# Performance work log

Measured on AMD Instinct MI355X. Metric: run time of the kernel, lower is better.

The kernel has to match this reference:

```python
import jax, jax.numpy as jnp
import numpy as np

# dims
B, N, D = 256, 77, 768     # batch, CLIP tokens, token dim
K, Dn, H = 16, 768, 8      # nodes, node dim, heads
HID, L = 512, 2            # edge-MLP hidden, num GNN layers


def setup_inputs() -> dict:
    key = jax.random.key(0)
    ks = jax.random.split(key, 12)
    g = lambda k, shape, s=0.02: (jax.random.normal(k, shape, jnp.float32) * s)
    return {
        "w": jax.random.normal(ks[0], (B, N, D), jnp.float32),
        "token_mask": jax.random.randint(ks[1], (B, N), 0, 2).astype(jnp.int32),
        "node_queries": g(ks[2], (1, K, Dn)),
        "Wq": g(ks[3], (Dn, Dn)), "bq": jnp.zeros((Dn,), jnp.float32),
        "Wk": g(ks[4], (D, Dn)),  "bk": jnp.zeros((Dn,), jnp.float32),
        "Wv": g(ks[5], (D, Dn)),  "bv": jnp.zeros((Dn,), jnp.float32),
        "We1": g(ks[6], (2 * Dn, HID)), "be1": jnp.zeros((HID,), jnp.float32),
        "We2": g(ks[7], (HID, 1)),      "be2": jnp.zeros((1,), jnp.float32),
        "fuse_gate": jnp.float32(0.0),
        "Wg": g(ks[8], (L, Dn, Dn)), "bg": jnp.zeros((L, Dn), jnp.float32),
    }


def _edge_logits(V, We1, be1, We2, be2):
    # edge_mlp(cat[Vi, Vj]) without materializing [B,K,K,2Dn]:
    # split first linear into the Vi-half and Vj-half of its weight.
    hi = V @ We1[:Dn]   # [B,K,HID]
    hj = V @ We1[Dn:]   # [B,K,HID]
    h = jax.nn.relu(hi[:, :, None, :] + hj[:, None, :, :] + be1)  # [B,K,K,HID]
    return jnp.einsum('bijh,h->bij', h, We2[:, 0]) + be2[0]       # [B,K,K]


def _forward(w, node_queries, Wq, bq, Wk, bk, Wv, bv,
             We1, be1, We2, be2, fuse_gate, Wg, bg, token_mask):
    q = jnp.broadcast_to(node_queries, (B, K, Dn))
    Q = q @ Wq + bq        # [B,K,Dn]
    Kt = w @ Wk + bk       # [B,N,Dn]
    Vt = w @ Wv + bv       # [B,N,Dn]
    # per-head dot products summed over heads == full Dn dot product
    scale = (Dn // H) ** -0.5
    scores = jnp.einsum('bkd,bnd->bkn', Q, Kt) * scale  # [B,K,N]
    pad = (token_mask == 0)[:, None, :]                 # [B,1,N]
    scores = jnp.where(pad, jnp.finfo(scores.dtype).min, scores)
    # softmax over K per token (transpose to [B,N,K])
    S = jax.nn.softmax(jnp.swapaxes(scores, 1, 2), axis=-1)  # [B,N,K]
    V = jnp.einsum('bnk,bnd->bkd', S, Vt)                    # [B,K,Dn]
    gate = jax.nn.sigmoid(fuse_gate)
    V = (1.0 - gate) * V + gate * q
    # pre-GNN edge logits, then relational GNN refinement
    E = _edge_logits(V, We1, be1, We2, be2)
    A = jax.nn.softmax(E, axis=-1)  # [B,K,K], fixed across layers
    for l in range(L):
        msg = jnp.einsum('bij,bjd->bid', A, V @ Wg[l] + bg[l])
        V = V + jax.nn.relu(msg)
    # post-GNN edge logits
    E = _edge_logits(V, We1, be1, We2, be2)
    return S, V, E


def reference(w, token_mask, node_queries, Wq, bq, Wk, bk, Wv, bv,
              We1, be1, We2, be2, fuse_gate, Wg, bg):
    return _forward(w, node_queries, Wq, bq, Wk, bk, Wv, bv,
                    We1, be1, We2, be2, fuse_gate, Wg, bg, token_mask)
```

## Files before the change

kernel.cpp:

```cpp
#include <hip/hip_runtime.h>

typedef unsigned short u16;
typedef __attribute__((ext_vector_type(8))) short short8;
typedef __attribute__((ext_vector_type(4))) float f32x4;

#define DEV static __device__ __forceinline__

DEV float bf2f(u16 u) { return __uint_as_float(((unsigned)u) << 16); }
DEV u16 f2bf(float f) {
  unsigned u = __float_as_uint(f);
  return (u16)((u + 0x7fffu + ((u >> 16) & 1u)) >> 16);
}

DEV void cp16(void* lds, const void* g) {
  __builtin_amdgcn_global_load_lds(
      (const __attribute__((address_space(1))) unsigned int*)g,
      (__attribute__((address_space(3))) unsigned int*)lds, 16, 0, 0);
}


__global__ __launch_bounds__(256) void tcast_all(const float* __restrict__ Wv,
                                                 const float* __restrict__ We1,
                                                 const float* __restrict__ Wg,
                                                 u16* __restrict__ WvT,
                                                 u16* __restrict__ We1T,
                                                 u16* __restrict__ WgT) {
  __shared__ float tile[32][33];
  const float* src; u16* dst; int C;
  switch (blockIdx.z) {
    case 0: src = Wv;           dst = WvT;           C = 768; break;
    case 1: src = We1;          dst = We1T;          C = 512; break;
    case 2: src = We1 + 393216; dst = We1T + 393216; C = 512; break;
    case 3: src = Wg;           dst = WgT;           C = 768; break;
    default: src = Wg + 589824; dst = WgT + 589824;  C = 768; break;
  }
  int r0 = blockIdx.y * 32, c0 = blockIdx.x * 32;
  if (c0 >= C) return;
  int tr = threadIdx.x >> 5, tc = threadIdx.x & 31;
#pragma unroll
  for (int rr = 0; rr < 4; ++rr)
    tile[tr + rr * 8][tc] = src[(size_t)(r0 + tr + rr * 8) * C + c0 + tc];
  __syncthreads();
#pragma unroll
  for (int rr = 0; rr < 4; ++rr)
    dst[(size_t)(c0 + tr + rr * 8) * 768 + r0 + tc] = f2bf(tile[tc][tr + rr * 8]);
}

__global__ __launch_bounds__(256) void q_part(const float* __restrict__ nq,
                                              const float* __restrict__ Wq,
                                              float* __restrict__ Qpart) {
  int gid = blockIdx.x * 256 + threadIdx.x;
  int s = blockIdx.y;
  int k = gid / 768, d = gid % 768;
  const float* nr = nq + k * 768 + s * 96;
  const float* wp = Wq + (size_t)(s * 96) * 768 + d;
  float s0 = 0.f, s1 = 0.f, s2 = 0.f, s3 = 0.f;
#pragma unroll
  for (int c = 0; c < 96; c += 4) {
    s0 += nr[c + 0] * wp[(size_t)(c + 0) * 768];
    s1 += nr[c + 1] * wp[(size_t)(c + 1) * 768];
    s2 += nr[c + 2] * wp[(size_t)(c + 2) * 768];
    s3 += nr[c + 3] * wp[(size_t)(c + 3) * 768];
  }
  Qpart[(size_t)s * 12288 + gid] = (s0 + s1) + (s2 + s3);
}

__global__ __launch_bounds__(256) void q_reduce(const float* __restrict__ Qpart,
                                                const float* __restrict__ bq,
                                                float* __restrict__ Qf) {
  int gid = blockIdx.x * 256 + threadIdx.x;
  int d = gid % 768;
  float s = bq[d];
#pragma unroll
  for (int i = 0; i < 8; ++i) s += Qpart[(size_t)i * 12288 + gid];
  Qf[gid] = s;
}

__global__ __launch_bounds__(256) void pt_kernel(const float* __restrict__ Qf,
                                                 const float* __restrict__ Wk,
                                                 const float* __restrict__ bk,
                                                 u16* __restrict__ PT16,
                                                 float* __restrict__ qb) {
  int t = threadIdx.x;
  if (blockIdx.x == 48) {
    int k = t >> 4, j = t & 15;
    const float* q = Qf + k * 768 + j * 48;
    const float* bp = bk + j * 48;
    float s = 0.f;
#pragma unroll
    for (int d = 0; d < 48; d += 4) {
      f32x4 qv = *(const f32x4*)&q[d];
      f32x4 bv4 = *(const f32x4*)&bp[d];
      s += qv[0] * bv4[0] + qv[1] * bv4[1] + qv[2] * bv4[2] + qv[3] * bv4[3];
    }
#pragma unroll
    for (int off = 1; off < 16; off <<= 1) s += __shfl_xor(s, off);
    if (j == 0) qb[k] = s;
    return;
  }
  int gid = blockIdx.x * 256 + t;
  int c = gid >> 4, k = gid & 15;
  const float* wr = Wk + (size_t)c * 768;
  const float* q = Qf + k * 768;
  float s = 0.f;
  for (int d = 0; d < 768; d += 4) {
    f32x4 wv = *(const f32x4*)&wr[d];
    f32x4 qv = *(const f32x4*)&q[d];
    s += wv[0] * qv[0] + wv[1] * qv[1] + wv[2] * qv[2] + wv[3] * qv[3];
  }
  PT16[k * 768 + c] = f2bf(s);
}

__global__ __launch_bounds__(256) void scoreu_kernel(const float* __restrict__ w,
                                                     const u16* __restrict__ PT16,
                                                     const float* __restrict__ qb,
                                                     const int* __restrict__ mask,
                                                     float* __restrict__ Sout,
                                                     u16* __restrict__ U16,
                                                     float* __restrict__ sk) {
  __shared__ u16 Ps[16 * 776];
  __shared__ float Ss[80 * 16];
  int b = blockIdx.x, t = threadIdx.x;
  int wave = t >> 6, lane = t & 63, l16 = lane & 15, quad = lane >> 4;
#pragma unroll
  for (int r = 0; r < 6; ++r) {
    int idx = t + 256 * r;
    int row = idx / 96, c8 = idx % 96;
    *(short8*)&Ps[row * 776 + c8 * 8] = *(const short8*)&PT16[row * 768 + c8 * 8];
  }
  __syncthreads();
  const float scale = 0.1020620726159658f;
  float qv = qb[l16];
  for (int tile = wave; tile < 5; tile += 4) {
    int nrow = tile * 16 + l16;
    int nclamp = nrow < 77 ? nrow : 76;
    const float* ap = w + ((size_t)b * 77 + nclamp) * 768 + quad * 8;
    f32x4 acc = {0.f, 0.f, 0.f, 0.f};
#pragma unroll
    for (int it = 0; it < 24; ++it) {
      f32x4 a0 = *(const f32x4*)(ap + it * 32);
      f32x4 a1 = *(const f32x4*)(ap + it * 32 + 4);
      short8 fa;
#pragma unroll
      for (int e = 0; e < 4; ++e) { fa[e] = (short)f2bf(a0[e]); fa[e + 4] = (short)f2bf(a1[e]); }
      short8 fb = *(const short8*)&Ps[l16 * 776 + it * 32 + quad * 8];
      acc = __builtin_amdgcn_mfma_f32_16x16x32_bf16(fa, fb, acc, 0, 0, 0);
    }
#pragma unroll
    for (int r = 0; r < 4; ++r) {
      int n_r = tile * 16 + quad * 4 + r;
      if (n_r < 77) {
        float s = (acc[r] + qv) * scale;
        if (mask[b * 77 + n_r] == 0) s = -3.402823466e38f;
        float mx = s;
#pragma unroll
        for (int off = 1; off < 16; off <<= 1) mx = fmaxf(mx, __shfl_xor(mx, off));
        float e = __expf(s - mx);
        float sm = e;
#pragma unroll
        for (int off = 1; off < 16; off <<= 1) sm += __shfl_xor(sm, off);
        float p = e / sm;
        Sout[((size_t)b * 77 + n_r) * 16 + l16] = p;
        Ss[n_r * 16 + l16] = p;
      }
    }
  }
  __syncthreads();
  float a0[16], a1[16], a2[16];
#pragma unroll
  for (int k = 0; k < 16; ++k) { a0[k] = 0.f; a1[k] = 0.f; a2[k] = 0.f; }
  const float* wb = w + (size_t)b * 59136;
  for (int n = 0; n < 77; ++n) {
    const float* wr = wb + (size_t)n * 768;
    float w0 = wr[t], w1 = wr[t + 256], w2 = wr[t + 512];
    const float* sr = &Ss[n * 16];
#pragma unroll
    for (int k = 0; k < 16; ++k) {
      float s = sr[k];
      a0[k] += s * w0; a1[k] += s * w1; a2[k] += s * w2;
    }
  }
  u16* ub = U16 + (size_t)b * 12288;
#pragma unroll
  for (int k = 0; k < 16; ++k) {
    ub[k * 768 + t] = f2bf(a0[k]);
    ub[k * 768 + t + 256] = f2bf(a1[k]);
    ub[k * 768 + t + 512] = f2bf(a2[k]);
  }
  if (t < 16) {
    float s = 0.f;
    for (int n = 0; n < 77; ++n) s += Ss[n * 16 + t];
    sk[b * 16 + t] = s;
  }
}

__global__ __launch_bounds__(256) void vgemm(const u16* __restrict__ A,
                                             const u16* __restrict__ BT,
                                             const float* __restrict__ skp,
                                             const float* __restrict__ bv,
                                             const float* __restrict__ nq,
                                             const float* __restrict__ gatep,
                                             float* __restrict__ V32,
                                             u16* __restrict__ V16) {
  __shared__ u16 As[2 * 64 * 32];
  __shared__ u16 Bs[2 * 128 * 32];
  int mi = blockIdx.x / 6, ni = blockIdx.x % 6;
  int m0 = mi * 64, n0 = ni * 128;
  int t = threadIdx.x;
  int wave = t >> 6, lane = t & 63, l16 = lane & 15, quad = lane >> 4;
  int ra = wave * 16 + (lane >> 2);
  int rb1 = wave * 32 + (lane >> 2);
  int rb2 = rb1 + 16;
  int cslot = lane & 3;
  int cga = (cslot ^ ((ra >> 1) & 3)) * 8;
  int cgb1 = (cslot ^ ((rb1 >> 1) & 3)) * 8;
  int cgb2 = (cslot ^ ((rb2 >> 1) & 3)) * 8;

  const u16* Ap = A + (size_t)(m0 + ra) * 768 + cga;
  const u16* Bp1 = BT + (size_t)(n0 + rb1) * 768 + cgb1;
  const u16* Bp2 = BT + (size_t)(n0 + rb2) * 768 + cgb2;
  u16* AsW = &As[(wave * 16) * 32];
  u16* BsW1 = &Bs[(wave * 32) * 32];
  u16* BsW2 = &Bs[(wave * 32 + 16) * 32];

  f32x4 zero4 = {0.f, 0.f, 0.f, 0.f};
  f32x4 acc[4][2];
#pragma unroll
  for (int i = 0; i < 4; ++i) { acc[i][0] = zero4; acc[i][1] = zero4; }

  cp16(AsW, Ap); cp16(BsW1, Bp1); cp16(BsW2, Bp2);

  int cur = 0;
  for (int k0 = 0; k0 < 768; k0 += 32) {
    int nxt = cur ^ 1;
    if (k0 + 32 < 768) {
      cp16(AsW + nxt * 2048, Ap + k0 + 32);
      cp16(BsW1 + nxt * 4096, Bp1 + k0 + 32);
      cp16(BsW2 + nxt * 4096, Bp2 + k0 + 32);
      asm volatile("s_waitcnt vmcnt(3)" ::: "memory");
    } else {
      asm volatile("s_waitcnt vmcnt(0)" ::: "memory");
    }
    asm volatile("s_barrier" ::: "memory");
    const u16* Ab = &As[cur * 2048];
    const u16* Bb = &Bs[cur * 4096];
    short8 fa[4], fb[2];
#pragma unroll
    for (int i = 0; i < 4; ++i) {
      int R = i * 16 + l16;
      fa[i] = *(const short8*)&Ab[R * 32 + (quad ^ ((R >> 1) & 3)) * 8];
    }
#pragma unroll
    for (int j = 0; j < 2; ++j) {
      int R = wave * 32 + j * 16 + l16;
      fb[j] = *(const short8*)&Bb[R * 32 + (quad ^ ((R >> 1) & 3)) * 8];
    }
#pragma unroll
    for (int i = 0; i < 4; ++i)
#pragma unroll
      for (int j = 0; j < 2; ++j)
        acc[i][j] = __builtin_amdgcn_mfma_f32_16x16x32_bf16(fa[i], fb[j], acc[i][j], 0, 0, 0);
    asm volatile("s_barrier" ::: "memory");
    cur = nxt;
  }

  float gv = gatep[0];
  float g = 1.f / (1.f + __expf(-gv)), og = 1.f - g;
  int narr[2]; float bvj[2];
#pragma unroll
  for (int j = 0; j < 2; ++j) {
    narr[j] = n0 + wave * 32 + j * 16 + l16;
    bvj[j] = bv[narr[j]];
  }
#pragma unroll
  for (int i = 0; i < 4; ++i)
#pragma unroll
    for (int r = 0; r < 4; ++r) {
      int m = m0 + i * 16 + quad * 4 + r;
      float skv = skp[m];
      size_t mrow = (size_t)m * 768;
      const float* nqr = nq + (m & 15) * 768;
#pragma unroll
      for (int j = 0; j < 2; ++j) {
        float val = acc[i][j][r] + skv * bvj[j];
        float v = og * val + g * nqr[narr[j]];
        V32[mrow + narr[j]] = v;
        V16[mrow + narr[j]] = f2bf(v);
      }
    }
}

__global__ __launch_bounds__(256) void gemm16s(const u16* __restrict__ A,
                                               const u16* __restrict__ BT0,
                                               const float* __restrict__ bias0,
                                               u16* __restrict__ C0, int N0, int ntA,
                                               const u16* __restrict__ BT1,
                                               const float* __restrict__ bias1,
                                               u16* __restrict__ C1, int N1, int ntB,
                                               int K) {
  __shared__ u16 As[2 * 64 * 32];
  __shared__ u16 Bs[2 * 128 * 32];
  int nt = ntA + ntB;
  int mi = blockIdx.x / nt, ni = blockIdx.x % nt;
  const u16* BT; const float* bias; u16* C; int N, n0;
  if (ni < ntA) { BT = BT0; bias = bias0; C = C0; N = N0; n0 = ni * 128; }
  else          { BT = BT1; bias = bias1; C = C1; N = N1; n0 = (ni - ntA) * 128; }
  int m0 = mi * 64;
  int t = threadIdx.x;
  int wave = t >> 6, lane = t & 63, l16 = lane & 15, quad = lane >> 4;
  int ra = wave * 16 + (lane >> 2);
  int rb1 = wave * 32 + (lane >> 2);
  int rb2 = rb1 + 16;
  int cslot = lane & 3;
  int cga = (cslot ^ ((ra >> 1) & 3)) * 8;
  int cgb1 = (cslot ^ ((rb1 >> 1) & 3)) * 8;
  int cgb2 = (cslot ^ ((rb2 >> 1) & 3)) * 8;

  const u16* Ap = A + (size_t)(m0 + ra) * K + cga;
  const u16* Bp1 = BT + (size_t)(n0 + rb1) * K + cgb1;
  const u16* Bp2 = BT + (size_t)(n0 + rb2) * K + cgb2;
  u16* AsW = &As[(wave * 16) * 32];
  u16* BsW1 = &Bs[(wave * 32) * 32];
  u16* BsW2 = &Bs[(wave * 32 + 16) * 32];

  f32x4 zero4 = {0.f, 0.f, 0.f, 0.f};
  f32x4 acc[4][2];
#pragma unroll
  for (int i = 0; i < 4; ++i) { acc[i][0] = zero4; acc[i][1] = zero4; }

  cp16(AsW, Ap); cp16(BsW1, Bp1); cp16(BsW2, Bp2);

  int cur = 0;
  for (int k0 = 0; k0 < K; k0 += 32) {
    int nxt = cur ^ 1;
    if (k0 + 32 < K) {
      cp16(AsW + nxt * 2048, Ap + k0 + 32);
      cp16(BsW1 + nxt * 4096, Bp1 + k0 + 32);
      cp16(BsW2 + nxt * 4096, Bp2 + k0 + 32);
      asm volatile("s_waitcnt vmcnt(3)" ::: "memory");
    } else {
      asm volatile("s_waitcnt vmcnt(0)" ::: "memory");
    }
    asm volatile("s_barrier" ::: "memory");
    const u16* Ab = &As[cur * 2048];
    const u16* Bb = &Bs[cur * 4096];
    short8 fa[4], fb[2];
#pragma unroll
    for (int i = 0; i < 4; ++i) {
      int R = i * 16 + l16;
      fa[i] = *(const short8*)&Ab[R * 32 + (quad ^ ((R >> 1) & 3)) * 8];
    }
#pragma unroll
    for (int j = 0; j < 2; ++j) {
      int R = wave * 32 + j * 16 + l16;
      fb[j] = *(const short8*)&Bb[R * 32 + (quad ^ ((R >> 1) & 3)) * 8];
    }
#pragma unroll
    for (int i = 0; i < 4; ++i)
#pragma unroll
      for (int j = 0; j < 2; ++j)
        acc[i][j] = __builtin_amdgcn_mfma_f32_16x16x32_bf16(fa[i], fb[j], acc[i][j], 0, 0, 0);
    asm volatile("s_barrier" ::: "memory");
    cur = nxt;
  }

  int narr[2]; float bvj[2];
#pragma unroll
  for (int j = 0; j < 2; ++j) {
    narr[j] = n0 + wave * 32 + j * 16 + l16;
    bvj[j] = bias ? bias[narr[j]] : 0.f;
  }
#pragma unroll
  for (int i = 0; i < 4; ++i)
#pragma unroll
    for (int r = 0; r < 4; ++r) {
      size_t mrow = (size_t)(m0 + i * 16 + quad * 4 + r) * N;
#pragma unroll
      for (int j = 0; j < 2; ++j)
        C[mrow + narr[j]] = f2bf(acc[i][j][r] + bvj[j]);
    }
}

__global__ __launch_bounds__(256) void edge_kernel(const u16* __restrict__ HIJ,
                                                   const float* __restrict__ be1,
                                                   const float* __restrict__ We2,
                                                   const float* __restrict__ be2v,
                                                   float* __restrict__ Aout,
                                                   float* __restrict__ Eout) {
  __shared__ float hiS[16 * 260];
  __shared__ float hjS[16 * 260];
  __shared__ float be1s[512];
  __shared__ float w2s[512];
  int b = blockIdx.x, t = threadIdx.x;
  be1s[t] = be1[t]; be1s[t + 256] = be1[t + 256];
  w2s[t] = We2[t];  w2s[t + 256] = We2[t + 256];

  int i = t >> 4, jj = t & 15;
  float e = 0.f;
  for (int half = 0; half < 2; ++half) {
    __syncthreads();
#pragma unroll
    for (int r = 0; r < 2; ++r) {
      int idx = t + 256 * r;
      int row = idx >> 5, c8 = idx & 31;
      const u16* src = &HIJ[(size_t)(b * 16 + row) * 1024 + half * 256 + c8 * 8];
      short8 hv = *(const short8*)src;
      short8 jv = *(const short8*)(src + 512);
      f32x4 l0, l1, m0v, m1v;
#pragma unroll
      for (int ee = 0; ee < 4; ++ee) {
        l0[ee] = bf2f((u16)hv[ee]); l1[ee] = bf2f((u16)hv[ee + 4]);
        m0v[ee] = bf2f((u16)jv[ee]); m1v[ee] = bf2f((u16)jv[ee + 4]);
      }
      *(f32x4*)&hiS[row * 260 + c8 * 8] = l0;
      *(f32x4*)&hiS[row * 260 + c8 * 8 + 4] = l1;
      *(f32x4*)&hjS[row * 260 + c8 * 8] = m0v;
      *(f32x4*)&hjS[row * 260 + c8 * 8 + 4] = m1v;
    }
    __syncthreads();
    const float* hi = &hiS[i * 260];
    const float* hj = &hjS[jj * 260];
    const float* b1 = &be1s[half * 256];
    const float* w2 = &w2s[half * 256];
#pragma unroll 2
    for (int h4 = 0; h4 < 64; ++h4) {
      f32x4 hv = *(const f32x4*)&hi[h4 * 4];
      f32x4 jv = *(const f32x4*)&hj[h4 * 4];
      f32x4 bv = *(const f32x4*)&b1[h4 * 4];
      f32x4 wv = *(const f32x4*)&w2[h4 * 4];
#pragma unroll
      for (int ee = 0; ee < 4; ++ee)
        e += fmaxf(hv[ee] + jv[ee] + bv[ee], 0.f) * wv[ee];
    }
  }
  e += be2v[0];

  if (Aout) {
    float mx = e;
#pragma unroll
    for (int off = 1; off < 16; off <<= 1) mx = fmaxf(mx, __shfl_xor(mx, off));
    float ex = __expf(e - mx);
    float sm = ex;
#pragma unroll
    for (int off = 1; off < 16; off <<= 1) sm += __shfl_xor(sm, off);
    Aout[(size_t)b * 256 + t] = ex / sm;
  }
  if (Eout) Eout[(size_t)b * 256 + t] = e;
}

__global__ __launch_bounds__(256) void edgecombine_kernel(const u16* __restrict__ HIJ,
                                                          const float* __restrict__ be1,
                                                          const float* __restrict__ We2,
                                                          const float* __restrict__ be2v,
                                                          float* __restrict__ Aout,
                                                          const u16* __restrict__ G,
                                                          float* __restrict__ V32,
                                                          u16* __restrict__ V16) {
  __shared__ float buf[16 * 772];
  __shared__ float be1s[512];
  __shared__ float w2s[512];
  __shared__ float As_s[256];
  float* hiS = buf;
  float* hjS = buf + 16 * 260;
  int b = blockIdx.x, t = threadIdx.x;
  be1s[t] = be1[t]; be1s[t + 256] = be1[t + 256];
  w2s[t] = We2[t];  w2s[t + 256] = We2[t + 256];

  int i = t >> 4, jj = t & 15;
  float e = 0.f;
  for (int half = 0; half < 2; ++half) {
    __syncthreads();
#pragma unroll
    for (int r = 0; r < 2; ++r) {
      int idx = t + 256 * r;
      int row = idx >> 5, c8 = idx & 31;
      const u16* src = &HIJ[(size_t)(b * 16 + row) * 1024 + half * 256 + c8 * 8];
      short8 hv = *(const short8*)src;
      short8 jv = *(const short8*)(src + 512);
      f32x4 l0, l1, m0v, m1v;
#pragma unroll
      for (int ee = 0; ee < 4; ++ee) {
        l0[ee] = bf2f((u16)hv[ee]); l1[ee] = bf2f((u16)hv[ee + 4]);
        m0v[ee] = bf2f((u16)jv[ee]); m1v[ee] = bf2f((u16)jv[ee + 4]);
      }
      *(f32x4*)&hiS[row * 260 + c8 * 8] = l0;
      *(f32x4*)&hiS[row * 260 + c8 * 8 + 4] = l1;
      *(f32x4*)&hjS[row * 260 + c8 * 8] = m0v;
      *(f32x4*)&hjS[row * 260 + c8 * 8 + 4] = m1v;
    }
    __syncthreads();
    const float* hi = &hiS[i * 260];
    const float* hj = &hjS[jj * 260];
    const float* b1 = &be1s[half * 256];
    const float* w2 = &w2s[half * 256];
#pragma unroll 2
    for (int h4 = 0; h4 < 64; ++h4) {
      f32x4 hv = *(const f32x4*)&hi[h4 * 4];
      f32x4 jv = *(const f32x4*)&hj[h4 * 4];
      f32x4 bv = *(const f32x4*)&b1[h4 * 4];
      f32x4 wv = *(const f32x4*)&w2[h4 * 4];
#pragma unroll
      for (int ee = 0; ee < 4; ++ee)
        e += fmaxf(hv[ee] + jv[ee] + bv[ee], 0.f) * wv[ee];
    }
  }
  e += be2v[0];

  float mx = e;
#pragma unroll
  for (int off = 1; off < 16; off <<= 1) mx = fmaxf(mx, __shfl_xor(mx, off));
  float ex = __expf(e - mx);
  float sm = ex;
#pragma unroll
  for (int off = 1; off < 16; off <<= 1) sm += __shfl_xor(sm, off);
  float p = ex / sm;
  As_s[t] = p;
  Aout[(size_t)b * 256 + t] = p;
  __syncthreads();

  float* Gs = buf;
#pragma unroll
  for (int r = 0; r < 6; ++r) {
    int idx = t + 256 * r;
    int row = idx / 96, c8 = idx % 96;
    short8 gv8 = *(const short8*)&G[(size_t)(b * 16 + row) * 768 + c8 * 8];
    f32x4 l0, l1;
#pragma unroll
    for (int ee = 0; ee < 4; ++ee) { l0[ee] = bf2f((u16)gv8[ee]); l1[ee] = bf2f((u16)gv8[ee + 4]); }
    *(f32x4*)&Gs[row * 772 + c8 * 8] = l0;
    *(f32x4*)&Gs[row * 772 + c8 * 8 + 4] = l1;
  }
  __syncthreads();
#pragma unroll
  for (int m = 0; m < 3; ++m) {
    int d = t + m * 256;
    float gv[16];
#pragma unroll
    for (int j = 0; j < 16; ++j) gv[j] = Gs[j * 772 + d];
#pragma unroll
    for (int ii = 0; ii < 16; ++ii) {
      float msg = 0.f;
#pragma unroll
      for (int j = 0; j < 16; ++j) msg += As_s[ii * 16 + j] * gv[j];
      size_t idx = (size_t)b * 12288 + (size_t)ii * 768 + d;
      float v = V32[idx] + fmaxf(msg, 0.f);
      V32[idx] = v;
      V16[idx] = f2bf(v);
    }
  }
}

__global__ __launch_bounds__(256) void combine_kernel(const float* __restrict__ Aws,
                                                      const u16* __restrict__ G,
                                                      float* __restrict__ V32,
                                                      u16* __restrict__ V16,
                                                      float* __restrict__ Vout) {
  __shared__ float Gs[16 * 772];
  __shared__ float As[256];
  int b = blockIdx.x, t = threadIdx.x;
#pragma unroll
  for (int r = 0; r < 6; ++r) {
    int idx = t + 256 * r;
    int row = idx / 96, c8 = idx % 96;
    short8 gv8 = *(const short8*)&G[(size_t)(b * 16 + row) * 768 + c8 * 8];
    f32x4 l0, l1;
#pragma unroll
    for (int ee = 0; ee < 4; ++ee) { l0[ee] = bf2f((u16)gv8[ee]); l1[ee] = bf2f((u16)gv8[ee + 4]); }
    *(f32x4*)&Gs[row * 772 + c8 * 8] = l0;
    *(f32x4*)&Gs[row * 772 + c8 * 8 + 4] = l1;
  }
  As[t] = Aws[(size_t)b * 256 + t];
  __syncthreads();
#pragma unroll
  for (int m = 0; m < 3; ++m) {
    int d = t + m * 256;
    float gv[16];
#pragma unroll
    for (int j = 0; j < 16; ++j) gv[j] = Gs[j * 772 + d];
#pragma unroll
    for (int i = 0; i < 16; ++i) {
      float msg = 0.f;
#pragma unroll
      for (int j = 0; j < 16; ++j) msg += As[i * 16 + j] * gv[j];
      size_t idx = (size_t)b * 12288 + (size_t)i * 768 + d;
      float v = V32[idx] + fmaxf(msg, 0.f);
      V32[idx] = v;
      V16[idx] = f2bf(v);
      if (Vout) Vout[idx] = v;
    }
  }
}

extern "C" void kernel_launch(void* const* d_in, const int* in_sizes, int n_in,
                              void* d_out, int out_size, void* d_ws, size_t ws_size,
                              hipStream_t stream) {
  const float* w    = (const float*)d_in[0];
  const int*   mask = (const int*)d_in[1];
  const float* nq   = (const float*)d_in[2];
  const float* Wq   = (const float*)d_in[3];
  const float* bq   = (const float*)d_in[4];
  const float* Wk   = (const float*)d_in[5];
  const float* bk   = (const float*)d_in[6];
  const float* Wv   = (const float*)d_in[7];
  const float* bv   = (const float*)d_in[8];
  const float* We1  = (const float*)d_in[9];
  const float* be1  = (const float*)d_in[10];
  const float* We2  = (const float*)d_in[11];
  const float* be2  = (const float*)d_in[12];
  const float* gate = (const float*)d_in[13];
  const float* Wg   = (const float*)d_in[14];
  const float* bg   = (const float*)d_in[15];

  float* ws    = (float*)d_ws;
  float* V32   = ws;
  float* Aws   = V32 + 3145728;
  float* Qpart = Aws + 65536;
  float* Qf    = Qpart + 98304;
  float* qb    = Qf + 12288;
  float* sk    = qb + 16;
  u16* PT16    = (u16*)(sk + 4096);
  u16* WvT     = PT16 + 12288;
  u16* We1T    = WvT + 589824;
  u16* WgT     = We1T + 786432;
  u16* V16     = WgT + 1179648;
  u16* U16     = V16 + 3145728;
  u16* HIJ     = U16 + 3145728;
  u16* Gws     = HIJ + 4194304;

  float* out  = (float*)d_out;
  float* Sout = out;
  float* Vout = out + 315392;
  float* Eout = out + 315392 + 3145728;

  dim3 blk(256);

  tcast_all<<<dim3(24, 24, 5), blk, 0, stream>>>(Wv, We1, Wg, WvT, We1T, WgT);
  q_part<<<dim3(48, 8), blk, 0, stream>>>(nq, Wq, Qpart);
  q_reduce<<<48, blk, 0, stream>>>(Qpart, bq, Qf);
  pt_kernel<<<49, blk, 0, stream>>>(Qf, Wk, bk, PT16, qb);

  scoreu_kernel<<<256, blk, 0, stream>>>(w, PT16, qb, mask, Sout, U16, sk);

  vgemm<<<384, blk, 0, stream>>>(U16, WvT, sk, bv, nq, gate, V32, V16);

  gemm16s<<<896, blk, 0, stream>>>(V16, We1T, nullptr, HIJ, 1024, 8,
                                   WgT, bg, Gws, 768, 6, 768);
  edgecombine_kernel<<<256, blk, 0, stream>>>(HIJ, be1, We2, be2, Aws, Gws, V32, V16);

  gemm16s<<<384, blk, 0, stream>>>(V16, WgT + 589824, bg + 768, Gws, 768, 6,
                                   WgT + 589824, bg + 768, Gws, 768, 0, 768);
  combine_kernel<<<256, blk, 0, stream>>>(Aws, Gws, V32, V16, Vout);

  gemm16s<<<512, blk, 0, stream>>>(V16, We1T, nullptr, HIJ, 1024, 8,
                                   We1T, nullptr, HIJ, 1024, 0, 768);
  edge_kernel<<<256, blk, 0, stream>>>(HIJ, be1, We2, be2, (float*)nullptr, Eout);
}
```

Baseline: 363.3 us.

## Split score/softmax and S^T·w into separate kernels; XCD-swizzle GEMM blocks

After: 337.2 us. -7.2%, faster.

```diff
diff --git a/kernel.cpp b/kernel.cpp
--- a/kernel.cpp
+++ b/kernel.cpp
@@ -16,6 +16,12 @@
   __builtin_amdgcn_global_load_lds(
       (const __attribute__((address_space(1))) unsigned int*)g,
       (__attribute__((address_space(3))) unsigned int*)lds, 16, 0, 0);
+}
+
+DEV int xcd_swz() {
+  int bid = blockIdx.x;
+  int cpx = gridDim.x >> 3;
+  return (bid & 7) * cpx + (bid >> 3);
 }
 
 
@@ -111,17 +117,14 @@
   PT16[k * 768 + c] = f2bf(s);
 }
 
-__global__ __launch_bounds__(256) void scoreu_kernel(const float* __restrict__ w,
-                                                     const u16* __restrict__ PT16,
-                                                     const float* __restrict__ qb,
-                                                     const int* __restrict__ mask,
-                                                     float* __restrict__ Sout,
-                                                     u16* __restrict__ U16,
-                                                     float* __restrict__ sk) {
+__global__ __launch_bounds__(256) void score2(const float* __restrict__ w,
+                                              const u16* __restrict__ PT16,
+                                              const float* __restrict__ qb,
+                                              const int* __restrict__ mask,
+                                              float* __restrict__ Sout) {
   __shared__ u16 Ps[16 * 776];
-  __shared__ float Ss[80 * 16];
-  int b = blockIdx.x, t = threadIdx.x;
-  int wave = t >> 6, lane = t & 63, l16 = lane & 15, quad = lane >> 4;
+  int t = threadIdx.x, wave = t >> 6, lane = t & 63, l16 = lane & 15, quad = lane >> 4;
+  int m0 = blockIdx.x * 64;
 #pragma unroll
   for (int r = 0; r < 6; ++r) {
     int idx = t + 256 * r;
@@ -129,65 +132,64 @@
     *(short8*)&Ps[row * 776 + c8 * 8] = *(const short8*)&PT16[row * 768 + c8 * 8];
   }
   __syncthreads();
+  int row = m0 + wave * 16 + l16;
+  const float* ap = w + (size_t)row * 768 + quad * 8;
+  f32x4 acc = {0.f, 0.f, 0.f, 0.f};
+#pragma unroll
+  for (int it = 0; it < 24; ++it) {
+    f32x4 a0 = *(const f32x4*)(ap + it * 32);
+    f32x4 a1 = *(const f32x4*)(ap + it * 32 + 4);
+    short8 fa;
+#pragma unroll
+    for (int e = 0; e < 4; ++e) { fa[e] = (short)f2bf(a0[e]); fa[e + 4] = (short)f2bf(a1[e]); }
+    short8 fb = *(const short8*)&Ps[l16 * 776 + it * 32 + quad * 8];
+    acc = __builtin_amdgcn_mfma_f32_16x16x32_bf16(fa, fb, acc, 0, 0, 0);
+  }
+  float qv = qb[l16];
   const float scale = 0.1020620726159658f;
-  float qv = qb[l16];
-  for (int tile = wave; tile < 5; tile += 4) {
-    int nrow = tile * 16 + l16;
-    int nclamp = nrow < 77 ? nrow : 76;
-    const float* ap = w + ((size_t)b * 77 + nclamp) * 768 + quad * 8;
-    f32x4 acc = {0.f, 0.f, 0.f, 0.f};
-#pragma unroll
-    for (int it = 0; it < 24; ++it) {
-      f32x4 a0 = *(const f32x4*)(ap + it * 32);
-      f32x4 a1 = *(const f32x4*)(ap + it * 32 + 4);
-      short8 fa;
-#pragma unroll
-      for (int e = 0; e < 4; ++e) { fa[e] = (short)f2bf(a0[e]); fa[e + 4] = (short)f2bf(a1[e]); }
-      short8 fb = *(const short8*)&Ps[l16 * 776 + it * 32 + quad * 8];
-      acc = __builtin_amdgcn_mfma_f32_16x16x32_bf16(fa, fb, acc, 0, 0, 0);
-    }
-#pragma unroll
-    for (int r = 0; r < 4; ++r) {
-      int n_r = tile * 16 + quad * 4 + r;
-      if (n_r < 77) {
-        float s = (acc[r] + qv) * scale;
-        if (mask[b * 77 + n_r] == 0) s = -3.402823466e38f;
-        float mx = s;
-#pragma unroll
-        for (int off = 1; off < 16; off <<= 1) mx = fmaxf(mx, __shfl_xor(mx, off));
-        float e = __expf(s - mx);
-        float sm = e;
-#pragma unroll
-        for (int off = 1; off < 16; off <<= 1) sm += __shfl_xor(sm, off);
-        float p = e / sm;
-        Sout[((size_t)b * 77 + n_r) * 16 + l16] = p;
-        Ss[n_r * 16 + l16] = p;
-      }
-    }
+#pragma unroll
+  for (int r = 0; r < 4; ++r) {
+    int orow = m0 + wave * 16 + quad * 4 + r;
+    float s = (acc[r] + qv) * scale;
+    if (mask[orow] == 0) s = -3.402823466e38f;
+    float mx = s;
+#pragma unroll
+    for (int off = 1; off < 16; off <<= 1) mx = fmaxf(mx, __shfl_xor(mx, off));
+    float e = __expf(s - mx);
+    float sm = e;
+#pragma unroll
+    for (int off = 1; off < 16; off <<= 1) sm += __shfl_xor(sm, off);
+    Sout[(size_t)orow * 16 + l16] = e / sm;
+  }
+}
+
+__global__ __launch_bounds__(256) void u_kernel(const float* __restrict__ Sg,
+                                                const float* __restrict__ w,
+                                                u16* __restrict__ U16,
+                                                float* __restrict__ sk) {
+  __shared__ float Ss[1232];
+  int b = blockIdx.x, t = threadIdx.x;
+  int d = blockIdx.y * 256 + t;
+#pragma unroll
+  for (int r = 0; r < 5; ++r) {
+    int idx = t + 256 * r;
+    if (idx < 1232) Ss[idx] = Sg[(size_t)b * 1232 + idx];
   }
   __syncthreads();
-  float a0[16], a1[16], a2[16];
-#pragma unroll
-  for (int k = 0; k < 16; ++k) { a0[k] = 0.f; a1[k] = 0.f; a2[k] = 0.f; }
-  const float* wb = w + (size_t)b * 59136;
+  float a[16];
+#pragma unroll
+  for (int k = 0; k < 16; ++k) a[k] = 0.f;
+  const float* wp = w + (size_t)b * 59136;
   for (int n = 0; n < 77; ++n) {
-    const float* wr = wb + (size_t)n * 768;
-    float w0 = wr[t], w1 = wr[t + 256], w2 = wr[t + 512];
+    float g = wp[(size_t)n * 768 + d];
     const float* sr = &Ss[n * 16];
 #pragma unroll
-    for (int k = 0; k < 16; ++k) {
-      float s = sr[k];
-      a0[k] += s * w0; a1[k] += s * w1; a2[k] += s * w2;
-    }
-  }
-  u16* ub = U16 + (size_t)b * 12288;
-#pragma unroll
-  for (int k = 0; k < 16; ++k) {
-    ub[k * 768 + t] = f2bf(a0[k]);
-    ub[k * 768 + t + 256] = f2bf(a1[k]);
-    ub[k * 768 + t + 512] = f2bf(a2[k]);
-  }
-  if (t < 16) {
+    for (int k = 0; k < 16; ++k) a[k] += sr[k] * g;
+  }
+#pragma unroll
+  for (int k = 0; k < 16; ++k)
+    U16[(size_t)b * 12288 + (size_t)k * 768 + d] = f2bf(a[k]);
+  if (blockIdx.y == 0 && t < 16) {
     float s = 0.f;
     for (int n = 0; n < 77; ++n) s += Ss[n * 16 + t];
     sk[b * 16 + t] = s;
@@ -204,7 +206,8 @@
                                              u16* __restrict__ V16) {
   __shared__ u16 As[2 * 64 * 32];
   __shared__ u16 Bs[2 * 128 * 32];
-  int mi = blockIdx.x / 6, ni = blockIdx.x % 6;
+  int swz = xcd_swz();
+  int mi = swz / 6, ni = swz % 6;
   int m0 = mi * 64, n0 = ni * 128;
   int t = threadIdx.x;
   int wave = t >> 6, lane = t & 63, l16 = lane & 15, quad = lane >> 4;
@@ -301,7 +304,8 @@
   __shared__ u16 As[2 * 64 * 32];
   __shared__ u16 Bs[2 * 128 * 32];
   int nt = ntA + ntB;
-  int mi = blockIdx.x / nt, ni = blockIdx.x % nt;
+  int swz = xcd_swz();
+  int mi = swz / nt, ni = swz % nt;
   const u16* BT; const float* bias; u16* C; int N, n0;
   if (ni < ntA) { BT = BT0; bias = bias0; C = C0; N = N0; n0 = ni * 128; }
   else          { BT = BT1; bias = bias1; C = C1; N = N1; n0 = (ni - ntA) * 128; }
@@ -639,8 +643,9 @@
   q_reduce<<<48, blk, 0, stream>>>(Qpart, bq, Qf);
   pt_kernel<<<49, blk, 0, stream>>>(Qf, Wk, bk, PT16, qb);
 
-  scoreu_kernel<<<256, blk, 0, stream>>>(w, PT16, qb, mask, Sout, U16, sk);
-
+  score2<<<308, blk, 0, stream>>>(w, PT16, qb, mask, Sout);
+
+  u_kernel<<<dim3(256, 3), blk, 0, stream>>>(Sout, w, U16, sk);
   vgemm<<<384, blk, 0, stream>>>(U16, WvT, sk, bv, nq, gate, V32, V16);
 
   gemm16s<<<896, blk, 0, stream>>>(V16, We1T, nullptr, HIJ, 1024, 8,
```
